# Kernel tuning notes

Hardware: AMD Instinct MI355X
Metric: run time of the kernel (lower is better)

The kernel has to match this reference:

```python
import jax, jax.numpy as jnp
import numpy as np

B, N, K = 2, 16384, 16
C_IN, C_OUT, SHARE = 64, 64, 8
ATTN = C_OUT // SHARE  # 8
EPS = 1e-5


def bn(x, gamma, beta):
    # BatchNorm2d_P: normalize over (B, N, K) per channel, training-mode batch stats
    m = jnp.mean(x, axis=(0, 1, 2), keepdims=True)
    v = jnp.var(x, axis=(0, 1, 2), keepdims=True)  # biased variance
    return (x - m) * jax.lax.rsqrt(v + EPS) * gamma + beta


def gather(points, idx):
    # points: (B, N, C), idx: (B, N, K) -> (B, N, K, C)
    b, n, k = idx.shape
    flat = idx.reshape(b, n * k)
    out = jnp.take_along_axis(points, flat[:, :, None], axis=1)
    return out.reshape(b, n, k, points.shape[-1])


def setup_inputs() -> dict:
    key = jax.random.key(0)
    ks = jax.random.split(key, 16)
    w = lambda k_, shp: (jax.random.normal(k_, shp, dtype=jnp.float32) * 0.02)
    inp = {
        "xyz": jax.random.normal(ks[0], (B, N, 3), dtype=jnp.float32),
        "features": jax.random.normal(ks[1], (B, N, C_IN), dtype=jnp.float32),
        "knn_idx": jax.random.randint(ks[2], (B, N, K), 0, N),
        "Wq": w(ks[3], (C_IN, C_OUT)), "bq": jnp.zeros((C_OUT,), jnp.float32),
        "Wk": w(ks[4], (C_IN, C_OUT)), "bk": jnp.zeros((C_OUT,), jnp.float32),
        "Wv": w(ks[5], (C_IN, C_OUT)), "bv": jnp.zeros((C_OUT,), jnp.float32),
        "Wd1": w(ks[6], (3, 3)), "bd1": jnp.zeros((3,), jnp.float32),
        "gamma_d": jnp.ones((3,), jnp.float32), "beta_d": jnp.zeros((3,), jnp.float32),
        "Wd2": w(ks[7], (3, C_OUT)), "bd2": jnp.zeros((C_OUT,), jnp.float32),
        "gamma_g1": jnp.ones((C_OUT,), jnp.float32), "beta_g1": jnp.zeros((C_OUT,), jnp.float32),
        "Wg1": w(ks[8], (C_OUT, ATTN)), "bg1": jnp.zeros((ATTN,), jnp.float32),
        "gamma_g2": jnp.ones((ATTN,), jnp.float32), "beta_g2": jnp.zeros((ATTN,), jnp.float32),
        "Wg2": w(ks[9], (ATTN, ATTN)), "bg2": jnp.zeros((ATTN,), jnp.float32),
    }
    return inp


def reference(xyz, features, knn_idx, Wq, bq, Wk, bk, Wv, bv,
              Wd1, bd1, gamma_d, beta_d, Wd2, bd2,
              gamma_g1, beta_g1, Wg1, bg1, gamma_g2, beta_g2, Wg2, bg2):
    q = features @ Wq + bq                       # (B,N,C_OUT)
    k = gather(features @ Wk + bk, knn_idx)      # (B,N,K,C_OUT)
    v = gather(features @ Wv + bv, knn_idx)      # (B,N,K,C_OUT)
    knn_xyz = gather(xyz, knn_idx)               # (B,N,K,3)
    rel = xyz[:, :, None, :] - knn_xyz           # (B,N,K,3)
    # fc_delta: Linear(3,3) -> BN -> ReLU -> Linear(3,C_OUT)
    pos_enc = jax.nn.relu(bn(rel @ Wd1 + bd1, gamma_d, beta_d)) @ Wd2 + bd2  # (B,N,K,C_OUT)
    # einops.reduce 'b n k (i j) -> b n k j' with j=mid_planes is identity (i=1)
    attn_in = q[:, :, None, :] - k + pos_enc     # (B,N,K,C_OUT)
    # fc_gamma: BN -> ReLU -> Linear(C_OUT,ATTN) -> BN -> ReLU -> Linear(ATTN,ATTN)
    h = jax.nn.relu(bn(attn_in, gamma_g1, beta_g1)) @ Wg1 + bg1  # (B,N,K,ATTN)
    h = jax.nn.relu(bn(h, gamma_g2, beta_g2)) @ Wg2 + bg2        # (B,N,K,ATTN)
    attn = jax.nn.softmax(h, axis=2)             # softmax over K neighbors
    vp = (v + pos_enc).reshape(B, N, K, SHARE, ATTN)
    res = jnp.einsum('bnksa,bnka->bnsa', vp, attn)
    return res.reshape(B, N, C_OUT)
```

## Files before the change

kernel.cpp:

```cpp
#include <hip/hip_runtime.h>
#include <hip/hip_bf16.h>

#define BB 2
#define NN 16384
#define KK 16
#define CC 64
#define AA 8
#define BN_PTS (BB*NN)
#define TOT (BB*NN*KK)
#define EPS 1e-5f

using bf = __hip_bfloat16;

__device__ __forceinline__ float ldf(const float* p, int i) { return p[i]; }
__device__ __forceinline__ float ldf(const bf* p, int i)    { return __bfloat162float(p[i]); }
__device__ __forceinline__ void  stf(float* p, int i, float v) { p[i] = v; }
__device__ __forceinline__ void  stf(bf* p, int i, float v)    { p[i] = __float2bfloat16(v); }

__device__ __forceinline__ float waveReduce(float v) {
    #pragma unroll
    for (int off = 32; off; off >>= 1) v += __shfl_down(v, off, 64);
    return v;
}

__global__ void detect_kernel(const unsigned* __restrict__ gbits, int* __restrict__ flag) {
    if (threadIdx.x == 0 && blockIdx.x == 0)
        *flag = (gbits[0] == 0x3F803F80u) ? 1 : 0;
}

template<typename T, int E>
__global__ __launch_bounds__(192) void qkv_kernel(
    const int* __restrict__ flag,
    const T* __restrict__ feat,
    const T* __restrict__ Wq, const T* __restrict__ bq,
    const T* __restrict__ Wk, const T* __restrict__ bk,
    const T* __restrict__ Wv, const T* __restrict__ bv,
    float* __restrict__ qf, float* __restrict__ kf, float* __restrict__ vf)
{
    if (*flag != E) return;
    __shared__ float fs[32*64];
    const int which = threadIdx.x / 64;
    const int c = threadIdx.x & 63;
    const T* W    = (which == 0) ? Wq : (which == 1) ? Wk : Wv;
    const T* bias = (which == 0) ? bq : (which == 1) ? bk : bv;
    float* out    = (which == 0) ? qf : (which == 1) ? kf : vf;

    float w[64];
    #pragma unroll
    for (int j = 0; j < 64; j++) w[j] = ldf(W, j*64 + c);
    const float bb_ = ldf(bias, c);

    const int row0 = blockIdx.x * 32;
    for (int i = threadIdx.x; i < 32*64; i += 192)
        fs[i] = ldf(feat, row0*64 + i);
    __syncthreads();

    for (int r = 0; r < 32; r++) {
        float acc = bb_;
        #pragma unroll
        for (int j = 0; j < 64; j++) acc = fmaf(fs[r*64 + j], w[j], acc);
        out[(row0 + r)*64 + c] = acc;
    }
}

template<typename T, int E>
__global__ __launch_bounds__(256) void statsd_kernel(
    const int* __restrict__ flag,
    const T* __restrict__ xyz, const int* __restrict__ knn,
    const T* __restrict__ Wd1, const T* __restrict__ bd1,
    float* __restrict__ part)
{
    if (*flag != E) return;
    float w[9], bi[3];
    #pragma unroll
    for (int i = 0; i < 9; i++) w[i] = ldf(Wd1, i);
    #pragma unroll
    for (int i = 0; i < 3; i++) bi[i] = ldf(bd1, i);

    float s[6] = {0,0,0,0,0,0};
    const int tid = blockIdx.x * 256 + threadIdx.x;
    for (int p = tid; p < TOT; p += 256*256) {
        const int bn = p >> 4;
        const int b  = bn >> 14;
        const int j  = knn[p];
        const int nb = (b << 14) + j;
        const float r0 = ldf(xyz, bn*3+0) - ldf(xyz, nb*3+0);
        const float r1 = ldf(xyz, bn*3+1) - ldf(xyz, nb*3+1);
        const float r2 = ldf(xyz, bn*3+2) - ldf(xyz, nb*3+2);
        const float d0 = fmaf(r0, w[0], fmaf(r1, w[3], fmaf(r2, w[6], bi[0])));
        const float d1 = fmaf(r0, w[1], fmaf(r1, w[4], fmaf(r2, w[7], bi[1])));
        const float d2 = fmaf(r0, w[2], fmaf(r1, w[5], fmaf(r2, w[8], bi[2])));
        s[0] += d0; s[1] += d1; s[2] += d2;
        s[3] = fmaf(d0, d0, s[3]); s[4] = fmaf(d1, d1, s[4]); s[5] = fmaf(d2, d2, s[5]);
    }
    __shared__ float red[4*6];
    const int lane = threadIdx.x & 63, wave = threadIdx.x >> 6;
    #pragma unroll
    for (int i = 0; i < 6; i++) {
        const float r = waveReduce(s[i]);
        if (lane == 0) red[wave*6 + i] = r;
    }
    __syncthreads();
    if (threadIdx.x < 6)
        part[blockIdx.x*8 + threadIdx.x] =
            red[threadIdx.x] + red[6+threadIdx.x] + red[12+threadIdx.x] + red[18+threadIdx.x];
}

template<typename T, int E>
__global__ void finalize_d(const int* __restrict__ flag,
                           const float* __restrict__ part,
                           const T* __restrict__ gamma, const T* __restrict__ beta,
                           float* __restrict__ coef)
{
    if (*flag != E) return;
    __shared__ float sums[6];
    const int t = threadIdx.x;
    if (t < 6) {
        float s = 0;
        for (int b = 0; b < 256; b++) s += part[b*8 + t];
        sums[t] = s;
    }
    __syncthreads();
    if (t < 3) {
        const float mean = sums[t] / (float)TOT;
        const float var  = sums[3+t] / (float)TOT - mean*mean;
        const float sc   = ldf(gamma, t) * rsqrtf(var + EPS);
        coef[t]   = sc;
        coef[4+t] = ldf(beta, t) - mean*sc;
    }
}

template<typename T, int E>
__global__ __launch_bounds__(256) void statsg1_kernel(
    const int* __restrict__ flag,
    const T* __restrict__ xyz, const int* __restrict__ knn,
    const float* __restrict__ qf, const float* __restrict__ kf,
    const T* __restrict__ Wd1, const T* __restrict__ bd1,
    const T* __restrict__ Wd2, const T* __restrict__ bd2,
    const float* __restrict__ coefd, float* __restrict__ part)
{
    if (*flag != E) return;
    const int lane = threadIdx.x & 63, wave = threadIdx.x >> 6;
    float w1[9], b1[3], sc[3], sh[3];
    #pragma unroll
    for (int i = 0; i < 9; i++) w1[i] = ldf(Wd1, i);
    #pragma unroll
    for (int i = 0; i < 3; i++) { b1[i] = ldf(bd1, i); sc[i] = coefd[i]; sh[i] = coefd[4+i]; }
    const float w2a = ldf(Wd2, lane), w2b = ldf(Wd2, 64+lane), w2c = ldf(Wd2, 128+lane);
    const float bd2c = ldf(bd2, lane);

    float sum = 0.f, sq = 0.f;
    for (int bn = blockIdx.x*4 + wave; bn < BN_PTS; bn += 2048*4) {
        const int b = bn >> 14;
        const float qv = qf[bn*64 + lane];
        const float x0 = ldf(xyz, bn*3+0), x1 = ldf(xyz, bn*3+1), x2 = ldf(xyz, bn*3+2);
        #pragma unroll
        for (int k = 0; k < 16; k++) {
            const int j  = knn[bn*16 + k];
            const int nb = (b << 14) + j;
            const float r0 = x0 - ldf(xyz, nb*3+0);
            const float r1 = x1 - ldf(xyz, nb*3+1);
            const float r2 = x2 - ldf(xyz, nb*3+2);
            float d0 = fmaf(r0, w1[0], fmaf(r1, w1[3], fmaf(r2, w1[6], b1[0])));
            float d1 = fmaf(r0, w1[1], fmaf(r1, w1[4], fmaf(r2, w1[7], b1[1])));
            float d2 = fmaf(r0, w1[2], fmaf(r1, w1[5], fmaf(r2, w1[8], b1[2])));
            d0 = fmaxf(fmaf(d0, sc[0], sh[0]), 0.f);
            d1 = fmaxf(fmaf(d1, sc[1], sh[1]), 0.f);
            d2 = fmaxf(fmaf(d2, sc[2], sh[2]), 0.f);
            const float pos = fmaf(d0, w2a, fmaf(d1, w2b, fmaf(d2, w2c, bd2c)));
            const float at = qv - kf[nb*64 + lane] + pos;
            sum += at; sq = fmaf(at, at, sq);
        }
    }
    __shared__ float ls[4][64], lq[4][64];
    ls[wave][lane] = sum; lq[wave][lane] = sq;
    __syncthreads();
    if (threadIdx.x < 64) {
        float a = 0.f, q = 0.f;
        #pragma unroll
        for (int w = 0; w < 4; w++) { a += ls[w][lane]; q += lq[w][lane]; }
        part[blockIdx.x*128 + lane]      = a;
        part[blockIdx.x*128 + 64 + lane] = q;
    }
}

template<int E>
__global__ __launch_bounds__(256) void reduce_g1(const int* __restrict__ flag,
                           const float* __restrict__ part, float* __restrict__ partB)
{
    if (*flag != E) return;
    __shared__ float red[2][128];
    const int t = threadIdx.x;
    const int col = t & 127, chunk = t >> 7;
    const int r0 = blockIdx.x * 32;
    float s = 0.f;
    #pragma unroll
    for (int j = 0; j < 16; j++) s += part[(r0 + chunk + 2*j)*128 + col];
    red[chunk][col] = s;
    __syncthreads();
    if (t < 128) partB[blockIdx.x*128 + t] = red[0][t] + red[1][t];
}

template<typename T, int E>
__global__ __launch_bounds__(512) void finalize_g1(const int* __restrict__ flag,
                            const float* __restrict__ partB,
                            const T* __restrict__ gamma, const T* __restrict__ beta,
                            float* __restrict__ coef)
{
    if (*flag != E) return;
    __shared__ float red[4][128];
    __shared__ float sums[128];
    const int t = threadIdx.x;
    const int col = t & 127, chunk = t >> 7;
    float s = 0.f;
    #pragma unroll
    for (int j = 0; j < 16; j++) s += partB[(chunk + 4*j)*128 + col];
    red[chunk][col] = s;
    __syncthreads();
    if (t < 128) sums[t] = red[0][t] + red[1][t] + red[2][t] + red[3][t];
    __syncthreads();
    if (t < 64) {
        const float mean = sums[t] / (float)TOT;
        const float var  = sums[64+t] / (float)TOT - mean*mean;
        const float sc   = ldf(gamma, t) * rsqrtf(var + EPS);
        coef[t]    = sc;
        coef[64+t] = ldf(beta, t) - mean*sc;
    }
}

#define H1_PAD 68
template<typename T, int E>
__global__ __launch_bounds__(256, 4) void h1_kernel(
    const int* __restrict__ flag,
    const T* __restrict__ xyz, const int* __restrict__ knn,
    const float* __restrict__ qf, const float* __restrict__ kf,
    const T* __restrict__ Wd1, const T* __restrict__ bd1,
    const T* __restrict__ Wd2, const T* __restrict__ bd2,
    const float* __restrict__ coefd, const float* __restrict__ coefg1,
    const T* __restrict__ Wg1, const T* __restrict__ bg1,
    float* __restrict__ h1, float* __restrict__ part)
{
    if (*flag != E) return;
    __shared__ float xs[128*H1_PAD];
    __shared__ float wg1s[512];
    __shared__ float ssum[4][8], ssq[4][8];
    const int t = threadIdx.x;
    const int lane = t & 63, wave = t >> 6;

    for (int i = t; i < 512; i += 256) wg1s[i] = ldf(Wg1, i);

    float w1[9], b1[3], scd[3], shd[3];
    #pragma unroll
    for (int i = 0; i < 9; i++) w1[i] = ldf(Wd1, i);
    #pragma unroll
    for (int i = 0; i < 3; i++) { b1[i] = ldf(bd1, i); scd[i] = coefd[i]; shd[i] = coefd[4+i]; }
    const float w2a = ldf(Wd2, lane), w2b = ldf(Wd2, 64+lane), w2c = ldf(Wd2, 128+lane);
    const float bd2c = ldf(bd2, lane);
    const float sc1 = coefg1[lane], sh1 = coefg1[64+lane];

    #pragma unroll
    for (int g = 0; g < 2; g++) {
        const int pl = wave*2 + g;
        const int bn = blockIdx.x*8 + pl;
        const int b  = bn >> 14;
        const float qv = qf[bn*64 + lane];
        const float x0 = ldf(xyz, bn*3+0), x1 = ldf(xyz, bn*3+1), x2 = ldf(xyz, bn*3+2);
        #pragma unroll
        for (int k = 0; k < 16; k++) {
            const int j  = knn[bn*16 + k];
            const int nb = (b << 14) + j;
            const float r0 = x0 - ldf(xyz, nb*3+0);
            const float r1 = x1 - ldf(xyz, nb*3+1);
            const float r2 = x2 - ldf(xyz, nb*3+2);
            float d0 = fmaf(r0, w1[0], fmaf(r1, w1[3], fmaf(r2, w1[6], b1[0])));
            float d1 = fmaf(r0, w1[1], fmaf(r1, w1[4], fmaf(r2, w1[7], b1[1])));
            float d2 = fmaf(r0, w1[2], fmaf(r1, w1[5], fmaf(r2, w1[8], b1[2])));
            d0 = fmaxf(fmaf(d0, scd[0], shd[0]), 0.f);
            d1 = fmaxf(fmaf(d1, scd[1], shd[1]), 0.f);
            d2 = fmaxf(fmaf(d2, scd[2], shd[2]), 0.f);
            const float pos = fmaf(d0, w2a, fmaf(d1, w2b, fmaf(d2, w2c, bd2c)));
            const float at = qv - kf[nb*64 + lane] + pos;
            xs[(pl*16 + k)*H1_PAD + lane] = fmaxf(fmaf(at, sc1, sh1), 0.f);
        }
    }
    __syncthreads();

    const int item = t >> 1;
    const int half = t & 1;
    float h[8];
    #pragma unroll
    for (int a = 0; a < 8; a++) h[a] = half ? 0.f : ldf(bg1, a);
    const float4* xr = (const float4*)(xs + item*H1_PAD) + half*8;
    const float* wbase = wg1s + half*256;
    #pragma unroll
    for (int cb = 0; cb < 8; cb++) {
        const float4 xv = xr[cb];
        #pragma unroll
        for (int jj = 0; jj < 4; jj++) {
            const float x = (jj == 0) ? xv.x : (jj == 1) ? xv.y : (jj == 2) ? xv.z : xv.w;
            const float4 wa = *(const float4*)&wbase[(cb*4 + jj)*8];
            const float4 wb = *(const float4*)&wbase[(cb*4 + jj)*8 + 4];
            h[0] = fmaf(x, wa.x, h[0]); h[1] = fmaf(x, wa.y, h[1]);
            h[2] = fmaf(x, wa.z, h[2]); h[3] = fmaf(x, wa.w, h[3]);
            h[4] = fmaf(x, wb.x, h[4]); h[5] = fmaf(x, wb.y, h[5]);
            h[6] = fmaf(x, wb.z, h[6]); h[7] = fmaf(x, wb.w, h[7]);
        }
    }
    #pragma unroll
    for (int a = 0; a < 8; a++) h[a] += __shfl_xor(h[a], 1, 64);

    const int it = blockIdx.x*128 + item;
    if (half == 0) {
        float4* hp = (float4*)(h1 + (size_t)it*8);
        hp[0] = make_float4(h[0], h[1], h[2], h[3]);
        hp[1] = make_float4(h[4], h[5], h[6], h[7]);
    }

    #pragma unroll
    for (int a = 0; a < 8; a++) {
        const float rs = waveReduce(h[a]);
        const float rq = waveReduce(h[a]*h[a]);
        if (lane == 0) { ssum[wave][a] = 0.5f*rs; ssq[wave][a] = 0.5f*rq; }
    }
    __syncthreads();
    if (t < 8) {
        part[blockIdx.x*16 + t]     = ssum[0][t] + ssum[1][t] + ssum[2][t] + ssum[3][t];
        part[blockIdx.x*16 + 8 + t] = ssq[0][t]  + ssq[1][t]  + ssq[2][t]  + ssq[3][t];
    }
}

template<int E>
__global__ __launch_bounds__(256) void reduce_g2(const int* __restrict__ flag,
                           const float* __restrict__ part, float* __restrict__ partB)
{
    if (*flag != E) return;
    __shared__ float red[16][16];
    const int t = threadIdx.x;
    const int col = t & 15, chunk = t >> 4;
    const int r0 = blockIdx.x * 64;
    float s = 0.f;
    #pragma unroll
    for (int j = 0; j < 4; j++) s += part[(r0 + chunk + 16*j)*16 + col];
    red[chunk][col] = s;
    __syncthreads();
    if (t < 16) {
        float a = 0.f;
        #pragma unroll
        for (int c = 0; c < 16; c++) a += red[c][t];
        partB[blockIdx.x*16 + t] = a;
    }
}

template<typename T, int E>
__global__ __launch_bounds__(256) void finalize_g2(const int* __restrict__ flag,
                            const float* __restrict__ partB,
                            const T* __restrict__ gamma, const T* __restrict__ beta,
                            float* __restrict__ coef)
{
    if (*flag != E) return;
    __shared__ float red[16][16];
    __shared__ float sums[16];
    const int t = threadIdx.x;
    const int col = t & 15, chunk = t >> 4;
    float s = 0.f;
    #pragma unroll
    for (int j = 0; j < 4; j++) s += partB[(chunk + 16*j)*16 + col];
    red[chunk][col] = s;
    __syncthreads();
    if (t < 16) {
        float a = 0.f;
        #pragma unroll
        for (int c = 0; c < 16; c++) a += red[c][t];
        sums[t] = a;
    }
    __syncthreads();
    if (t < 8) {
        const float mean = sums[t] / (float)TOT;
        const float var  = sums[8+t] / (float)TOT - mean*mean;
        const float sc   = ldf(gamma, t) * rsqrtf(var + EPS);
        coef[t]   = sc;
        coef[8+t] = ldf(beta, t) - mean*sc;
    }
}

template<typename T, int E>
__global__ __launch_bounds__(256) void out_kernel(
    const int* __restrict__ flag,
    const T* __restrict__ xyz, const int* __restrict__ knn,
    const float* __restrict__ vf, const float* __restrict__ h1,
    const T* __restrict__ Wd1, const T* __restrict__ bd1,
    const T* __restrict__ Wd2, const T* __restrict__ bd2,
    const float* __restrict__ coefd, const float* __restrict__ coefg2,
    const T* __restrict__ Wg2, const T* __restrict__ bg2,
    T* __restrict__ out)
{
    if (*flag != E) return;
    __shared__ float g[4][128];
    __shared__ float hh[4][128];
    __shared__ float dd[4][16][3];
    __shared__ int   idxs[4][16];
    __shared__ float wg2[64];
    const int t = threadIdx.x;
    const int bn0 = blockIdx.x * 4;

    if (t < 64) wg2[t] = ldf(Wg2, t);

    {
        const int p = t >> 6, f = t & 63;
        const int base = (bn0 + p) * 128;
        #pragma unroll
        for (int i = 0; i < 2; i++) {
            const int ff = f + i*64;
            const int a = ff & 7;
            const float v = h1[base + ff];
            g[p][ff] = fmaxf(fmaf(v, coefg2[a], coefg2[8 + a]), 0.f);
        }
    }
    if (t < 64) {
        const int p = t >> 4, k = t & 15;
        const int bn = bn0 + p;
        const int b = bn >> 14;
        const int j = knn[bn*16 + k];
        idxs[p][k] = j;
        const int nb = (b << 14) + j;
        const float r0 = ldf(xyz, bn*3+0) - ldf(xyz, nb*3+0);
        const float r1 = ldf(xyz, bn*3+1) - ldf(xyz, nb*3+1);
        const float r2 = ldf(xyz, bn*3+2) - ldf(xyz, nb*3+2);
        float d0 = fmaf(r0, ldf(Wd1,0), fmaf(r1, ldf(Wd1,3), fmaf(r2, ldf(Wd1,6), ldf(bd1,0))));
        float d1 = fmaf(r0, ldf(Wd1,1), fmaf(r1, ldf(Wd1,4), fmaf(r2, ldf(Wd1,7), ldf(bd1,1))));
        float d2 = fmaf(r0, ldf(Wd1,2), fmaf(r1, ldf(Wd1,5), fmaf(r2, ldf(Wd1,8), ldf(bd1,2))));
        dd[p][k][0] = fmaxf(fmaf(d0, coefd[0], coefd[4]), 0.f);
        dd[p][k][1] = fmaxf(fmaf(d1, coefd[1], coefd[5]), 0.f);
        dd[p][k][2] = fmaxf(fmaf(d2, coefd[2], coefd[6]), 0.f);
    }
    __syncthreads();

    {
        #pragma unroll
        for (int i = 0; i < 2; i++) {
            const int o = t + i*256;
            const int p = o >> 7, f = o & 127;
            const int a = f & 7, k = f >> 3;
            float acc = ldf(bg2, a);
            #pragma unroll
            for (int jj = 0; jj < 8; jj++) acc = fmaf(g[p][k*8 + jj], wg2[jj*8 + a], acc);
            hh[p][f] = acc;
        }
    }
    __syncthreads();

    if (t < 32) {
        const int p = t >> 3, a = t & 7;
        float m = -1e30f;
        #pragma unroll
        for (int k = 0; k < 16; k++) m = fmaxf(m, hh[p][k*8 + a]);
        float e[16]; float s = 0.f;
        #pragma unroll
        for (int k = 0; k < 16; k++) { e[k] = __expf(hh[p][k*8 + a] - m); s += e[k]; }
        const float inv = 1.f / s;
        #pragma unroll
        for (int k = 0; k < 16; k++) hh[p][k*8 + a] = e[k] * inv;
    }
    __syncthreads();

    {
        const int p = t >> 6, c = t & 63, a = c & 7;
        const int bn = bn0 + p;
        const int b = bn >> 14;
        const float w0 = ldf(Wd2, c), w1 = ldf(Wd2, 64 + c), w2 = ldf(Wd2, 128 + c);
        const float bd2c = ldf(bd2, c);
        float acc = 0.f;
        #pragma unroll
        for (int k = 0; k < 16; k++) {
            const int j = idxs[p][k];
            const float pos = fmaf(dd[p][k][0], w0, fmaf(dd[p][k][1], w1, fmaf(dd[p][k][2], w2, bd2c)));
            const float vv = vf[((b << 14) + j)*64 + c] + pos;
            acc = fmaf(vv, hh[p][k*8 + a], acc);
        }
        stf(out, bn*64 + c, acc);
    }
}

template<typename T, int E>
static void launch_all(void* const* d_in, void* d_out, float* ws, const int* flag,
                       hipStream_t stream) {
    const T*   xyz   = (const T*) d_in[0];
    const T*   feat  = (const T*) d_in[1];
    const int* knn   = (const int*)d_in[2];
    const T*   Wq    = (const T*) d_in[3];
    const T*   bq    = (const T*) d_in[4];
    const T*   Wk    = (const T*) d_in[5];
    const T*   bk    = (const T*) d_in[6];
    const T*   Wv    = (const T*) d_in[7];
    const T*   bv    = (const T*) d_in[8];
    const T*   Wd1   = (const T*) d_in[9];
    const T*   bd1   = (const T*) d_in[10];
    const T*   gd    = (const T*) d_in[11];
    const T*   betad = (const T*) d_in[12];
    const T*   Wd2   = (const T*) d_in[13];
    const T*   bd2   = (const T*) d_in[14];
    const T*   gg1   = (const T*) d_in[15];
    const T*   bg1b  = (const T*) d_in[16];
    const T*   Wg1   = (const T*) d_in[17];
    const T*   bg1   = (const T*) d_in[18];
    const T*   gg2   = (const T*) d_in[19];
    const T*   bg2b  = (const T*) d_in[20];
    const T*   Wg2   = (const T*) d_in[21];
    const T*   bg2   = (const T*) d_in[22];
    T* out = (T*)d_out;

    float* qf      = ws;
    float* kf      = ws + 2097152;
    float* vf      = ws + 4194304;
    float* h1      = ws + 6291456;
    float* part_d  = ws + 10485760;
    float* partA   = ws + 10487808;
    float* partB   = ws + 10749952;
    float* coef_d  = ws + 10758144;
    float* coef_g1 = ws + 10758152;
    float* coef_g2 = ws + 10758280;

    qkv_kernel<T,E><<<1024, 192, 0, stream>>>(flag, feat, Wq, bq, Wk, bk, Wv, bv, qf, kf, vf);
    statsd_kernel<T,E><<<256, 256, 0, stream>>>(flag, xyz, knn, Wd1, bd1, part_d);
    finalize_d<T,E><<<1, 64, 0, stream>>>(flag, part_d, gd, betad, coef_d);
    statsg1_kernel<T,E><<<2048, 256, 0, stream>>>(flag, xyz, knn, qf, kf, Wd1, bd1, Wd2, bd2,
                                                  coef_d, partA);
    reduce_g1<E><<<64, 256, 0, stream>>>(flag, partA, partB);
    finalize_g1<T,E><<<1, 512, 0, stream>>>(flag, partB, gg1, bg1b, coef_g1);
    h1_kernel<T,E><<<4096, 256, 0, stream>>>(flag, xyz, knn, qf, kf, Wd1, bd1, Wd2, bd2,
                                             coef_d, coef_g1, Wg1, bg1, h1, partA);
    reduce_g2<E><<<64, 256, 0, stream>>>(flag, partA, partB);
    finalize_g2<T,E><<<1, 256, 0, stream>>>(flag, partB, gg2, bg2b, coef_g2);
    out_kernel<T,E><<<8192, 256, 0, stream>>>(flag, xyz, knn, vf, h1, Wd1, bd1, Wd2, bd2,
                                              coef_d, coef_g2, Wg2, bg2, out);
}

extern "C" void kernel_launch(void* const* d_in, const int* in_sizes, int n_in,
                              void* d_out, int out_size, void* d_ws, size_t ws_size,
                              hipStream_t stream) {
    float* ws = (float*)d_ws;
    int* flag = (int*)(ws + 10758296);

    detect_kernel<<<1, 1, 0, stream>>>((const unsigned*)d_in[11], flag);

    launch_all<float, 0>(d_in, d_out, ws, flag, stream);
    launch_all<bf,    1>(d_in, d_out, ws, flag, stream);
}
```

Measured before the change: 285.8 us.

## Materialize pos-delta and bf16 attention inputs to skip recomputation in later passes

When the workspace is large enough, statsd stores the first-layer delta projections per neighbor and statsg1 stores the attention input as bf16. A new h1_fast kernel then streams those bf16 values instead of re-gathering xyz and k features, and out_kernel reads the stored deltas. The h1 shared-memory layout also gets a slot offset meant to avoid bank conflicts. This replaces recomputation and random gathers with large sequential writes and reads, and bf16 storage of activations adds rounding error before the BN and linear layers.

```diff
diff --git a/kernel.cpp b/kernel.cpp
--- a/kernel.cpp
+++ b/kernel.cpp
@@ -68,7 +68,8 @@
     const int* __restrict__ flag,
     const T* __restrict__ xyz, const int* __restrict__ knn,
     const T* __restrict__ Wd1, const T* __restrict__ bd1,
-    float* __restrict__ part)
+    float* __restrict__ part,
+    float* __restrict__ dx, float* __restrict__ dy, float* __restrict__ dz)
 {
     if (*flag != E) return;
     float w[9], bi[3];
@@ -90,6 +91,7 @@
         const float d0 = fmaf(r0, w[0], fmaf(r1, w[3], fmaf(r2, w[6], bi[0])));
         const float d1 = fmaf(r0, w[1], fmaf(r1, w[4], fmaf(r2, w[7], bi[1])));
         const float d2 = fmaf(r0, w[2], fmaf(r1, w[5], fmaf(r2, w[8], bi[2])));
+        if (dx) { dx[p] = d0; dy[p] = d1; dz[p] = d2; }
         s[0] += d0; s[1] += d1; s[2] += d2;
         s[3] = fmaf(d0, d0, s[3]); s[4] = fmaf(d1, d1, s[4]); s[5] = fmaf(d2, d2, s[5]);
     }
@@ -137,7 +139,9 @@
     const float* __restrict__ qf, const float* __restrict__ kf,
     const T* __restrict__ Wd1, const T* __restrict__ bd1,
     const T* __restrict__ Wd2, const T* __restrict__ bd2,
-    const float* __restrict__ coefd, float* __restrict__ part)
+    const float* __restrict__ coefd, float* __restrict__ part,
+    const float* __restrict__ dx, const float* __restrict__ dy,
+    const float* __restrict__ dz, bf* __restrict__ aibuf)
 {
     if (*flag != E) return;
     const int lane = threadIdx.x & 63, wave = threadIdx.x >> 6;
@@ -153,22 +157,30 @@
     for (int bn = blockIdx.x*4 + wave; bn < BN_PTS; bn += 2048*4) {
         const int b = bn >> 14;
         const float qv = qf[bn*64 + lane];
-        const float x0 = ldf(xyz, bn*3+0), x1 = ldf(xyz, bn*3+1), x2 = ldf(xyz, bn*3+2);
+        float x0 = 0.f, x1 = 0.f, x2 = 0.f;
+        if (!dx) { x0 = ldf(xyz, bn*3+0); x1 = ldf(xyz, bn*3+1); x2 = ldf(xyz, bn*3+2); }
         #pragma unroll
         for (int k = 0; k < 16; k++) {
-            const int j  = knn[bn*16 + k];
+            const int it = bn*16 + k;
+            const int j  = knn[it];
             const int nb = (b << 14) + j;
-            const float r0 = x0 - ldf(xyz, nb*3+0);
-            const float r1 = x1 - ldf(xyz, nb*3+1);
-            const float r2 = x2 - ldf(xyz, nb*3+2);
-            float d0 = fmaf(r0, w1[0], fmaf(r1, w1[3], fmaf(r2, w1[6], b1[0])));
-            float d1 = fmaf(r0, w1[1], fmaf(r1, w1[4], fmaf(r2, w1[7], b1[1])));
-            float d2 = fmaf(r0, w1[2], fmaf(r1, w1[5], fmaf(r2, w1[8], b1[2])));
+            float d0, d1, d2;
+            if (dx) {
+                d0 = dx[it]; d1 = dy[it]; d2 = dz[it];
+            } else {
+                const float r0 = x0 - ldf(xyz, nb*3+0);
+                const float r1 = x1 - ldf(xyz, nb*3+1);
+                const float r2 = x2 - ldf(xyz, nb*3+2);
+                d0 = fmaf(r0, w1[0], fmaf(r1, w1[3], fmaf(r2, w1[6], b1[0])));
+                d1 = fmaf(r0, w1[1], fmaf(r1, w1[4], fmaf(r2, w1[7], b1[1])));
+                d2 = fmaf(r0, w1[2], fmaf(r1, w1[5], fmaf(r2, w1[8], b1[2])));
+            }
             d0 = fmaxf(fmaf(d0, sc[0], sh[0]), 0.f);
             d1 = fmaxf(fmaf(d1, sc[1], sh[1]), 0.f);
             d2 = fmaxf(fmaf(d2, sc[2], sh[2]), 0.f);
             const float pos = fmaf(d0, w2a, fmaf(d1, w2b, fmaf(d2, w2c, bd2c)));
             const float at = qv - kf[nb*64 + lane] + pos;
+            if (aibuf) aibuf[(size_t)it*64 + lane] = __float2bfloat16(at);
             sum += at; sq = fmaf(at, at, sq);
         }
     }
@@ -225,6 +237,63 @@
         const float sc   = ldf(gamma, t) * rsqrtf(var + EPS);
         coef[t]    = sc;
         coef[64+t] = ldf(beta, t) - mean*sc;
+    }
+}
+
+template<typename T, int E>
+__global__ __launch_bounds__(256) void h1_fast(
+    const int* __restrict__ flag,
+    const unsigned* __restrict__ aibuf,
+    const float* __restrict__ coefg1,
+    const T* __restrict__ Wg1, const T* __restrict__ bg1,
+    float* __restrict__ h1, float* __restrict__ part)
+{
+    if (*flag != E) return;
+    __shared__ float wg1s[512];
+    __shared__ float scs[64], shs[64];
+    __shared__ float ssum[4][8], ssq[4][8];
+    const int t = threadIdx.x, lane = t & 63, wave = t >> 6;
+    for (int i = t; i < 512; i += 256) wg1s[i] = ldf(Wg1, i);
+    if (t < 64) { scs[t] = coefg1[t]; shs[t] = coefg1[64 + t]; }
+    __syncthreads();
+
+    const size_t item = (size_t)blockIdx.x*256 + t;
+    const uint4* src = (const uint4*)aibuf + item*8;
+    float h[8];
+    #pragma unroll
+    for (int a = 0; a < 8; a++) h[a] = ldf(bg1, a);
+    #pragma unroll
+    for (int cb = 0; cb < 8; cb++) {
+        const uint4 u = src[cb];
+        const unsigned uu[4] = {u.x, u.y, u.z, u.w};
+        #pragma unroll
+        for (int q = 0; q < 4; q++) {
+            const int c0 = cb*8 + q*2;
+            const float xlo = __uint_as_float(uu[q] << 16);
+            const float xhi = __uint_as_float(uu[q] & 0xffff0000u);
+            const float g0 = fmaxf(fmaf(xlo, scs[c0],   shs[c0]),   0.f);
+            const float g1 = fmaxf(fmaf(xhi, scs[c0+1], shs[c0+1]), 0.f);
+            #pragma unroll
+            for (int a = 0; a < 8; a++) {
+                h[a] = fmaf(g0, wg1s[c0*8 + a], h[a]);
+                h[a] = fmaf(g1, wg1s[(c0+1)*8 + a], h[a]);
+            }
+        }
+    }
+    float4* hp = (float4*)(h1 + item*8);
+    hp[0] = make_float4(h[0], h[1], h[2], h[3]);
+    hp[1] = make_float4(h[4], h[5], h[6], h[7]);
+
+    #pragma unroll
+    for (int a = 0; a < 8; a++) {
+        const float rs = waveReduce(h[a]);
+        const float rq = waveReduce(h[a]*h[a]);
+        if (lane == 0) { ssum[wave][a] = rs; ssq[wave][a] = rq; }
+    }
+    __syncthreads();
+    if (t < 8) {
+        part[blockIdx.x*16 + t]     = ssum[0][t] + ssum[1][t] + ssum[2][t] + ssum[3][t];
+        part[blockIdx.x*16 + 8 + t] = ssq[0][t]  + ssq[1][t]  + ssq[2][t]  + ssq[3][t];
     }
 }
 
@@ -257,6 +326,7 @@
     const float w2a = ldf(Wd2, lane), w2b = ldf(Wd2, 64+lane), w2c = ldf(Wd2, 128+lane);
     const float bd2c = ldf(bd2, lane);
     const float sc1 = coefg1[lane], sh1 = coefg1[64+lane];
+    const int lslot = (lane < 32) ? lane : lane + 4;
 
     #pragma unroll
     for (int g = 0; g < 2; g++) {
@@ -280,7 +350,7 @@
             d2 = fmaxf(fmaf(d2, scd[2], shd[2]), 0.f);
             const float pos = fmaf(d0, w2a, fmaf(d1, w2b, fmaf(d2, w2c, bd2c)));
             const float at = qv - kf[nb*64 + lane] + pos;
-            xs[(pl*16 + k)*H1_PAD + lane] = fmaxf(fmaf(at, sc1, sh1), 0.f);
+            xs[(pl*16 + k)*H1_PAD + lslot] = fmaxf(fmaf(at, sc1, sh1), 0.f);
         }
     }
     __syncthreads();
@@ -290,7 +360,7 @@
     float h[8];
     #pragma unroll
     for (int a = 0; a < 8; a++) h[a] = half ? 0.f : ldf(bg1, a);
-    const float4* xr = (const float4*)(xs + item*H1_PAD) + half*8;
+    const float4* xr = (const float4*)(xs + item*H1_PAD + half*36);
     const float* wbase = wg1s + half*256;
     #pragma unroll
     for (int cb = 0; cb < 8; cb++) {
@@ -331,16 +401,17 @@
 
 template<int E>
 __global__ __launch_bounds__(256) void reduce_g2(const int* __restrict__ flag,
-                           const float* __restrict__ part, float* __restrict__ partB)
+                           const float* __restrict__ part, float* __restrict__ partB,
+                           int rows)
 {
     if (*flag != E) return;
     __shared__ float red[16][16];
     const int t = threadIdx.x;
     const int col = t & 15, chunk = t >> 4;
-    const int r0 = blockIdx.x * 64;
+    const int rpb = rows >> 6;
+    const int r0 = blockIdx.x * rpb;
     float s = 0.f;
-    #pragma unroll
-    for (int j = 0; j < 4; j++) s += part[(r0 + chunk + 16*j)*16 + col];
+    for (int r = chunk; r < rpb; r += 16) s += part[(r0 + r)*16 + col];
     red[chunk][col] = s;
     __syncthreads();
     if (t < 16) {
@@ -392,6 +463,8 @@
     const T* __restrict__ Wd2, const T* __restrict__ bd2,
     const float* __restrict__ coefd, const float* __restrict__ coefg2,
     const T* __restrict__ Wg2, const T* __restrict__ bg2,
+    const float* __restrict__ dx, const float* __restrict__ dy,
+    const float* __restrict__ dz,
     T* __restrict__ out)
 {
     if (*flag != E) return;
@@ -420,15 +493,21 @@
         const int p = t >> 4, k = t & 15;
         const int bn = bn0 + p;
         const int b = bn >> 14;
-        const int j = knn[bn*16 + k];
+        const int it = bn*16 + k;
+        const int j = knn[it];
         idxs[p][k] = j;
-        const int nb = (b << 14) + j;
-        const float r0 = ldf(xyz, bn*3+0) - ldf(xyz, nb*3+0);
-        const float r1 = ldf(xyz, bn*3+1) - ldf(xyz, nb*3+1);
-        const float r2 = ldf(xyz, bn*3+2) - ldf(xyz, nb*3+2);
-        float d0 = fmaf(r0, ldf(Wd1,0), fmaf(r1, ldf(Wd1,3), fmaf(r2, ldf(Wd1,6), ldf(bd1,0))));
-        float d1 = fmaf(r0, ldf(Wd1,1), fmaf(r1, ldf(Wd1,4), fmaf(r2, ldf(Wd1,7), ldf(bd1,1))));
-        float d2 = fmaf(r0, ldf(Wd1,2), fmaf(r1, ldf(Wd1,5), fmaf(r2, ldf(Wd1,8), ldf(bd1,2))));
+        float d0, d1, d2;
+        if (dx) {
+            d0 = dx[it]; d1 = dy[it]; d2 = dz[it];
+        } else {
+            const int nb = (b << 14) + j;
+            const float r0 = ldf(xyz, bn*3+0) - ldf(xyz, nb*3+0);
+            const float r1 = ldf(xyz, bn*3+1) - ldf(xyz, nb*3+1);
+            const float r2 = ldf(xyz, bn*3+2) - ldf(xyz, nb*3+2);
+            d0 = fmaf(r0, ldf(Wd1,0), fmaf(r1, ldf(Wd1,3), fmaf(r2, ldf(Wd1,6), ldf(bd1,0))));
+            d1 = fmaf(r0, ldf(Wd1,1), fmaf(r1, ldf(Wd1,4), fmaf(r2, ldf(Wd1,7), ldf(bd1,1))));
+            d2 = fmaf(r0, ldf(Wd1,2), fmaf(r1, ldf(Wd1,5), fmaf(r2, ldf(Wd1,8), ldf(bd1,2))));
+        }
         dd[p][k][0] = fmaxf(fmaf(d0, coefd[0], coefd[4]), 0.f);
         dd[p][k][1] = fmaxf(fmaf(d1, coefd[1], coefd[5]), 0.f);
         dd[p][k][2] = fmaxf(fmaf(d2, coefd[2], coefd[6]), 0.f);
@@ -481,9 +560,11 @@
     }
 }
 
+#define WS_BIG_FLOATS 29108384ull
+
 template<typename T, int E>
 static void launch_all(void* const* d_in, void* d_out, float* ws, const int* flag,
-                       hipStream_t stream) {
+                       bool big, hipStream_t stream) {
     const T*   xyz   = (const T*) d_in[0];
     const T*   feat  = (const T*) d_in[1];
     const int* knn   = (const int*)d_in[2];
@@ -519,20 +600,30 @@
     float* coef_d  = ws + 10758144;
     float* coef_g1 = ws + 10758152;
     float* coef_g2 = ws + 10758280;
+    float* dx      = big ? ws + 10758304 : nullptr;
+    float* dy      = big ? ws + 11282592 : nullptr;
+    float* dz      = big ? ws + 11806880 : nullptr;
+    bf*    aibuf   = big ? (bf*)(ws + 12331168) : nullptr;
 
     qkv_kernel<T,E><<<1024, 192, 0, stream>>>(flag, feat, Wq, bq, Wk, bk, Wv, bv, qf, kf, vf);
-    statsd_kernel<T,E><<<256, 256, 0, stream>>>(flag, xyz, knn, Wd1, bd1, part_d);
+    statsd_kernel<T,E><<<256, 256, 0, stream>>>(flag, xyz, knn, Wd1, bd1, part_d, dx, dy, dz);
     finalize_d<T,E><<<1, 64, 0, stream>>>(flag, part_d, gd, betad, coef_d);
     statsg1_kernel<T,E><<<2048, 256, 0, stream>>>(flag, xyz, knn, qf, kf, Wd1, bd1, Wd2, bd2,
-                                                  coef_d, partA);
+                                                  coef_d, partA, dx, dy, dz, aibuf);
     reduce_g1<E><<<64, 256, 0, stream>>>(flag, partA, partB);
     finalize_g1<T,E><<<1, 512, 0, stream>>>(flag, partB, gg1, bg1b, coef_g1);
-    h1_kernel<T,E><<<4096, 256, 0, stream>>>(flag, xyz, knn, qf, kf, Wd1, bd1, Wd2, bd2,
-                                             coef_d, coef_g1, Wg1, bg1, h1, partA);
-    reduce_g2<E><<<64, 256, 0, stream>>>(flag, partA, partB);
+    if (big) {
+        h1_fast<T,E><<<2048, 256, 0, stream>>>(flag, (const unsigned*)aibuf, coef_g1,
+                                               Wg1, bg1, h1, partA);
+        reduce_g2<E><<<64, 256, 0, stream>>>(flag, partA, partB, 2048);
+    } else {
+        h1_kernel<T,E><<<4096, 256, 0, stream>>>(flag, xyz, knn, qf, kf, Wd1, bd1, Wd2, bd2,
+                                                 coef_d, coef_g1, Wg1, bg1, h1, partA);
+        reduce_g2<E><<<64, 256, 0, stream>>>(flag, partA, partB, 4096);
+    }
     finalize_g2<T,E><<<1, 256, 0, stream>>>(flag, partB, gg2, bg2b, coef_g2);
     out_kernel<T,E><<<8192, 256, 0, stream>>>(flag, xyz, knn, vf, h1, Wd1, bd1, Wd2, bd2,
-                                              coef_d, coef_g2, Wg2, bg2, out);
+                                              coef_d, coef_g2, Wg2, bg2, dx, dy, dz, out);
 }
 
 extern "C" void kernel_launch(void* const* d_in, const int* in_sizes, int n_in,
@@ -540,9 +631,10 @@
                               hipStream_t stream) {
     float* ws = (float*)d_ws;
     int* flag = (int*)(ws + 10758296);
+    const bool big = ws_size >= WS_BIG_FLOATS * 4ull;
 
     detect_kernel<<<1, 1, 0, stream>>>((const unsigned*)d_in[11], flag);
 
-    launch_all<float, 0>(d_in, d_out, ws, flag, stream);
-    launch_all<bf,    1>(d_in, d_out, ws, flag, stream);
-}
+    launch_all<float, 0>(d_in, d_out, ws, flag, big, stream);
+    launch_all<bf,    1>(d_in, d_out, ws, flag, big, stream);
+}
```

After: 277.6 us. 1.03x faster.
